# Optimization experiments

Hardware: AMD Instinct MI355X
Metric: run time of the kernel (lower is better)

## Reference

```python
import jax, jax.numpy as jnp
import numpy as np

V, E = 100000, 128
B, Q, D = 512, 32, 256
K_NUM, SIGMA, EXACT_SIGMA = 21, 0.1, 0.001
EPS = 1e-8


def _kernel_params():
    # faithful to source (including the sigma/exact_sigma swap at the call site)
    l_mu = [1.0]
    bin_size = 2.0 / (K_NUM - 1)
    l_mu.append(1 - bin_size / 2)
    for j in range(1, K_NUM - 1):
        l_mu.append(l_mu[j] - bin_size)
    mus = sorted(l_mu)
    # kernel_sigmas(n, sigma=exact_sigma, exact_sigma=sigma) due to swapped call
    sig_list = [SIGMA] + [EXACT_SIGMA] * (K_NUM - 1)
    sigmas = sorted(sig_list)[::-1]
    return (jnp.asarray(mus, dtype=jnp.float32),
            jnp.asarray(sigmas, dtype=jnp.float32))

MUS, SIGMAS = _kernel_params()


def setup_inputs() -> dict:
    key = jax.random.key(0)
    ks = jax.random.split(key, 11)
    emb = jax.random.normal(ks[0], (V, E), dtype=jnp.float32)
    emb = emb.at[0].set(0.0)  # padding_idx=0
    w1 = jax.random.normal(ks[1], (K_NUM, 10), dtype=jnp.float32) / np.sqrt(K_NUM)
    b1 = jax.random.normal(ks[2], (10,), dtype=jnp.float32) * 0.01
    w2 = jax.random.normal(ks[3], (10, 5), dtype=jnp.float32) / np.sqrt(10)
    b2 = jax.random.normal(ks[4], (5,), dtype=jnp.float32) * 0.01
    w3 = jax.random.normal(ks[5], (5, 1), dtype=jnp.float32) / np.sqrt(5)
    b3 = jax.random.normal(ks[6], (1,), dtype=jnp.float32) * 0.01
    query1 = jax.random.randint(ks[7], (B, Q), 0, V, dtype=jnp.int64 if jax.config.jax_enable_x64 else jnp.int32)
    doc1 = jax.random.randint(ks[8], (B, D), 0, V, dtype=query1.dtype)
    query2 = jax.random.randint(ks[9], (B, Q), 0, V, dtype=query1.dtype)
    doc2 = jax.random.randint(ks[10], (B, D), 0, V, dtype=query1.dtype)
    return {"emb": emb, "w1": w1, "b1": b1, "w2": w2, "b2": b2,
            "w3": w3, "b3": b3, "query1": query1, "doc1": doc1,
            "query2": query2, "doc2": doc2}


def _l2norm(x):
    n = jnp.linalg.norm(x, axis=-1, keepdims=True)
    return x / jnp.maximum(n, EPS)


def _predict(emb, w1, b1, w2, b2, w3, b3, q_idx, d_idx):
    q_idx = jnp.clip(q_idx, 0, V - 1)
    d_idx = jnp.clip(d_idx, 0, V - 1)
    qn = _l2norm(emb[q_idx])            # [B,Q,E]
    dn = _l2norm(emb[d_idx])            # [B,D,E]
    mm = jnp.einsum('bqe,bde->bqd', qn, dn)  # cosine matching matrix [B,Q,D]
    # soft-histogram Gaussian kernel pooling: [B,Q,D,K]
    phi = jnp.exp(-0.5 * (mm[..., None] - MUS) ** 2 / SIGMAS ** 2)
    k_out = jnp.log1p(phi.sum(axis=2)).sum(axis=1)  # [B,K]
    x = jax.nn.relu(k_out) @ w1 + b1
    x = jax.nn.relu(x) @ w2 + b2
    x = jax.nn.relu(x) @ w3 + b3
    return x  # [B,1]


def reference(emb, w1, b1, w2, b2, w3, b3, query1, doc1, query2, doc2):
    logits_1 = _predict(emb, w1, b1, w2, b2, w3, b3, query1, doc1)
    logits_2 = _predict(emb, w1, b1, w2, b2, w3, b3, query2, doc2)
    return jax.nn.sigmoid(logits_1 - logits_2)
```

## Files before the change

kernel.cpp:

```cpp
#include <hip/hip_runtime.h>
#include <math.h>

#define V_SIZE 100000
#define E_DIM  128
#define B_SIZE 512
#define Q_LEN  32
#define D_LEN  256
#define K_NUM  21


typedef _Float16 half8_t  __attribute__((ext_vector_type(8)));
typedef float    float4_t __attribute__((ext_vector_type(4)));

__global__ __launch_bounds__(256, 4) void knrm_main(
    const float* __restrict__ emb,
    const int* __restrict__ q1, const int* __restrict__ d1,
    const int* __restrict__ q2, const int* __restrict__ d2,
    const float* __restrict__ w1, const float* __restrict__ b1,
    const float* __restrict__ w2, const float* __restrict__ b2,
    const float* __restrict__ w3, const float* __restrict__ b3,
    float* __restrict__ logits)
{
    const int b    = blockIdx.x;
    const int pair = blockIdx.y;
    const int t    = threadIdx.x;
    const int* __restrict__ qidx = pair ? q2 : q1;
    const int* __restrict__ didx = pair ? d2 : d1;

    __shared__ half8_t AfH[2][4][64];
    __shared__ half8_t AfL[2][4][64];
    __shared__ float rnq[Q_LEN];
    __shared__ float phis[Q_LEN][22];
    __shared__ float ko[K_NUM];

    const int lane = t & 63;
    const int w    = t >> 6;
    const int quad = lane >> 4;
    const int l15  = lane & 15;

    for (int i = t; i < Q_LEN * 22; i += 256) ((float*)phis)[i] = 0.f;

    {
        const int qr = t >> 3;
        const int qc = t & 7;
        int qi = qidx[b * Q_LEN + qr];
        qi = min(max(qi, 0), V_SIZE - 1);
        const float4* src = (const float4*)(emb + (size_t)qi * E_DIM) + qc * 4;
        float4 v0 = src[0], v1 = src[1], v2 = src[2], v3 = src[3];
        float fv[16] = {v0.x,v0.y,v0.z,v0.w, v1.x,v1.y,v1.z,v1.w,
                        v2.x,v2.y,v2.z,v2.w, v3.x,v3.y,v3.z,v3.w};
        float ss = 0.f;
        half8_t h0, h1, l0, l1;
        #pragma unroll
        for (int j = 0; j < 8; ++j) {
            ss = fmaf(fv[j], fv[j], ss);
            _Float16 h = (_Float16)fv[j];
            h0[j] = h; l0[j] = (_Float16)(fv[j] - (float)h);
        }
        #pragma unroll
        for (int j = 0; j < 8; ++j) {
            ss = fmaf(fv[8 + j], fv[8 + j], ss);
            _Float16 h = (_Float16)fv[8 + j];
            h1[j] = h; l1[j] = (_Float16)(fv[8 + j] - (float)h);
        }
        const int qt  = qr >> 4;
        const int lr  = qr & 15;
        const int s   = qc >> 1;
        const int qd0 = (qc & 1) * 2;
        AfH[qt][s][qd0 * 16 + lr]       = h0;
        AfH[qt][s][(qd0 + 1) * 16 + lr] = h1;
        AfL[qt][s][qd0 * 16 + lr]       = l0;
        AfL[qt][s][(qd0 + 1) * 16 + lr] = l1;
        ss += __shfl_xor(ss, 1, 8);
        ss += __shfl_xor(ss, 2, 8);
        ss += __shfl_xor(ss, 4, 8);
        if (qc == 0) rnq[qr] = 1.0f / fmaxf(sqrtf(ss), 1e-8f);
    }
    __syncthreads();

    float rnqv[8];
    #pragma unroll
    for (int i = 0; i < 8; ++i) rnqv[i] = rnq[(i >> 2) * 16 + quad * 4 + (i & 3)];

    const float cc0 = -0.5f / (0.1f * 0.1f);
    const float ccs = -0.5f / (0.001f * 0.001f);
    float breg[8] = {0.f,0.f,0.f,0.f,0.f,0.f,0.f,0.f};

    int dix[4];
    #pragma unroll
    for (int c = 0; c < 4; ++c) {
        int di = didx[b * D_LEN + w * 64 + c * 16 + l15];
        dix[c] = min(max(di, 0), V_SIZE - 1);
    }

    half8_t bh[4], bl[4];
    float rnd;

    auto convert = [&](const float4* v) {
        float ss = 0.f;
        #pragma unroll
        for (int s = 0; s < 4; ++s) {
            float f[8] = {v[2*s].x, v[2*s].y, v[2*s].z, v[2*s].w,
                          v[2*s+1].x, v[2*s+1].y, v[2*s+1].z, v[2*s+1].w};
            half8_t h, l;
            #pragma unroll
            for (int j = 0; j < 8; ++j) {
                ss = fmaf(f[j], f[j], ss);
                _Float16 hh = (_Float16)f[j];
                h[j] = hh; l[j] = (_Float16)(f[j] - (float)hh);
            }
            bh[s] = h; bl[s] = l;
        }
        ss += __shfl_xor(ss, 16);
        ss += __shfl_xor(ss, 32);
        rnd = 1.0f / fmaxf(sqrtf(ss), 1e-8f);
    };

    {
        const float4* dr = (const float4*)(emb + (size_t)dix[0] * E_DIM) + quad * 2;
        float4 cur[8];
        #pragma unroll
        for (int s = 0; s < 4; ++s) { cur[2*s] = dr[s*8]; cur[2*s+1] = dr[s*8+1]; }
        convert(cur);
    }

    #pragma unroll
    for (int c = 0; c < 4; ++c) {
        float4 nx[8];
        if (c < 3) {
            const float4* dr = (const float4*)(emb + (size_t)dix[c+1] * E_DIM) + quad * 2;
            #pragma unroll
            for (int s = 0; s < 4; ++s) { nx[2*s] = dr[s*8]; nx[2*s+1] = dr[s*8+1]; }
        }

        float4_t acc0 = {0.f,0.f,0.f,0.f}, acc1 = {0.f,0.f,0.f,0.f};
        #pragma unroll
        for (int s = 0; s < 4; ++s) {
            half8_t a0h = AfH[0][s][lane], a0l = AfL[0][s][lane];
            half8_t a1h = AfH[1][s][lane], a1l = AfL[1][s][lane];
            acc0 = __builtin_amdgcn_mfma_f32_16x16x32_f16(a0h, bh[s], acc0, 0, 0, 0);
            acc1 = __builtin_amdgcn_mfma_f32_16x16x32_f16(a1h, bh[s], acc1, 0, 0, 0);
            acc0 = __builtin_amdgcn_mfma_f32_16x16x32_f16(a0l, bh[s], acc0, 0, 0, 0);
            acc1 = __builtin_amdgcn_mfma_f32_16x16x32_f16(a1l, bh[s], acc1, 0, 0, 0);
            acc0 = __builtin_amdgcn_mfma_f32_16x16x32_f16(a0h, bl[s], acc0, 0, 0, 0);
            acc1 = __builtin_amdgcn_mfma_f32_16x16x32_f16(a1h, bl[s], acc1, 0, 0, 0);
        }

        #pragma unroll
        for (int qt = 0; qt < 2; ++qt) {
            const float4_t acc = qt ? acc1 : acc0;
            #pragma unroll
            for (int r = 0; r < 4; ++r) {
                const float mm = acc[r] * rnqv[qt*4 + r] * rnd;
                const float x0 = mm + 0.95f;
                breg[qt*4 + r] += __expf(x0 * x0 * cc0);
                float g = rintf((mm + 0.85f) * 10.f);
                g = fminf(fmaxf(g, 0.f), 18.f);
                float mu = fmaf(g, 0.1f, -0.85f);
                int ks = (int)g + 1;
                if (mm > 0.975f) { mu = 1.0f; ks = 20; }
                const float xs = mm - mu;
                const float es = __expf(xs * xs * ccs);
                if (es > 0.f) atomicAdd(&phis[qt*16 + quad*4 + r][ks], es);
            }
        }

        if (c < 3) convert(nx);
    }

    #pragma unroll
    for (int i = 0; i < 8; ++i) {
        float v = breg[i];
        v += __shfl_xor(v, 1, 16);
        v += __shfl_xor(v, 2, 16);
        v += __shfl_xor(v, 4, 16);
        v += __shfl_xor(v, 8, 16);
        if (l15 == 0) atomicAdd(&phis[(i >> 2) * 16 + quad * 4 + (i & 3)][0], v);
    }
    __syncthreads();

    for (int p = t; p < K_NUM * Q_LEN; p += 256) {
        const int q = p & 31;
        const int k = p >> 5;
        float l = log1pf(phis[q][k]);
        l += __shfl_xor(l, 1, 32);
        l += __shfl_xor(l, 2, 32);
        l += __shfl_xor(l, 4, 32);
        l += __shfl_xor(l, 8, 32);
        l += __shfl_xor(l, 16, 32);
        if (q == 0) ko[k] = l;
    }
    __syncthreads();

    if (t == 0) {
        float x1v[10];
        #pragma unroll
        for (int i = 0; i < 10; ++i) {
            float s = b1[i];
            for (int k = 0; k < K_NUM; ++k) {
                float v = ko[k] > 0.f ? ko[k] : 0.f;
                s = fmaf(v, w1[k * 10 + i], s);
            }
            x1v[i] = s;
        }
        float x2v[5];
        #pragma unroll
        for (int i = 0; i < 5; ++i) {
            float s = b2[i];
            #pragma unroll
            for (int k = 0; k < 10; ++k) {
                float v = x1v[k] > 0.f ? x1v[k] : 0.f;
                s = fmaf(v, w2[k * 5 + i], s);
            }
            x2v[i] = s;
        }
        float s3 = b3[0];
        #pragma unroll
        for (int k = 0; k < 5; ++k) {
            float v = x2v[k] > 0.f ? x2v[k] : 0.f;
            s3 = fmaf(v, w3[k], s3);
        }
        logits[pair * B_SIZE + b] = s3;
    }
}

__global__ void knrm_final(const float* __restrict__ logits, float* __restrict__ out)
{
    const int b = blockIdx.x * blockDim.x + threadIdx.x;
    if (b < B_SIZE) {
        const float dl = logits[b] - logits[B_SIZE + b];
        out[b] = 1.0f / (1.0f + __expf(-dl));
    }
}

extern "C" void kernel_launch(void* const* d_in, const int* in_sizes, int n_in,
                              void* d_out, int out_size, void* d_ws, size_t ws_size,
                              hipStream_t stream)
{
    const float* emb = (const float*)d_in[0];
    const float* w1  = (const float*)d_in[1];
    const float* b1  = (const float*)d_in[2];
    const float* w2  = (const float*)d_in[3];
    const float* b2  = (const float*)d_in[4];
    const float* w3  = (const float*)d_in[5];
    const float* b3  = (const float*)d_in[6];
    const int*   q1  = (const int*)d_in[7];
    const int*   d1  = (const int*)d_in[8];
    const int*   q2  = (const int*)d_in[9];
    const int*   d2  = (const int*)d_in[10];

    float* logits = (float*)d_ws;
    float* out    = (float*)d_out;

    dim3 grid(B_SIZE, 2);
    knrm_main<<<grid, 256, 0, stream>>>(emb, q1, d1, q2, d2,
                                        w1, b1, w2, b2, w3, b3, logits);
    knrm_final<<<(B_SIZE + 255) / 256, 256, 0, stream>>>(logits, out);
}
```

Measured before the change: 124.9 us.

## Fuse both pairs and the sigmoid into one 512-thread kernel

Merges the two per-pair blocks into a single 512-thread block per batch row, so that both logits are computed together and the sigmoid difference is applied in-kernel. This removes the second kernel launch and the round trip through the logits workspace. It also issues the query and first document embedding gathers before the LDS zeroing and conversion, which lets the gather latency overlap with setup work. In exchange the block needs twice the shared memory and threads, which may reduce scheduling flexibility and occupancy.

```diff
diff --git a/kernel.cpp b/kernel.cpp
--- a/kernel.cpp
+++ b/kernel.cpp
@@ -12,41 +12,57 @@
 typedef _Float16 half8_t  __attribute__((ext_vector_type(8)));
 typedef float    float4_t __attribute__((ext_vector_type(4)));
 
-__global__ __launch_bounds__(256, 4) void knrm_main(
+__global__ __launch_bounds__(512, 4) void knrm_fused(
     const float* __restrict__ emb,
     const int* __restrict__ q1, const int* __restrict__ d1,
     const int* __restrict__ q2, const int* __restrict__ d2,
     const float* __restrict__ w1, const float* __restrict__ b1,
     const float* __restrict__ w2, const float* __restrict__ b2,
     const float* __restrict__ w3, const float* __restrict__ b3,
-    float* __restrict__ logits)
+    float* __restrict__ out)
 {
     const int b    = blockIdx.x;
-    const int pair = blockIdx.y;
     const int t    = threadIdx.x;
+    const int tl   = t & 255;
+    const int pair = t >> 8;
+
     const int* __restrict__ qidx = pair ? q2 : q1;
     const int* __restrict__ didx = pair ? d2 : d1;
 
-    __shared__ half8_t AfH[2][4][64];
-    __shared__ half8_t AfL[2][4][64];
-    __shared__ float rnq[Q_LEN];
-    __shared__ float phis[Q_LEN][22];
-    __shared__ float ko[K_NUM];
+    __shared__ half8_t AfH[2][2][4][64];
+    __shared__ half8_t AfL[2][2][4][64];
+    __shared__ float rnq[2][Q_LEN];
+    __shared__ float phis[2][Q_LEN][22];
+    __shared__ float ko[2][K_NUM];
+    __shared__ float logitL[2];
 
     const int lane = t & 63;
-    const int w    = t >> 6;
+    const int w    = tl >> 6;
     const int quad = lane >> 4;
     const int l15  = lane & 15;
 
-    for (int i = t; i < Q_LEN * 22; i += 256) ((float*)phis)[i] = 0.f;
+    const int qr = tl >> 3;
+    const int qc = tl & 7;
+    int qi = qidx[b * Q_LEN + qr];
+    int dix[4];
+    #pragma unroll
+    for (int c = 0; c < 4; ++c) {
+        int di = didx[b * D_LEN + w * 64 + c * 16 + l15];
+        dix[c] = min(max(di, 0), V_SIZE - 1);
+    }
+    qi = min(max(qi, 0), V_SIZE - 1);
+
+    const float4* src = (const float4*)(emb + (size_t)qi * E_DIM) + qc * 4;
+    float4 v0 = src[0], v1 = src[1], v2 = src[2], v3 = src[3];
+
+    const float4* dr0 = (const float4*)(emb + (size_t)dix[0] * E_DIM) + quad * 2;
+    float4 cur[8];
+    #pragma unroll
+    for (int s = 0; s < 4; ++s) { cur[2*s] = dr0[s*8]; cur[2*s+1] = dr0[s*8+1]; }
+
+    for (int i = tl; i < Q_LEN * 22; i += 256) ((float*)phis[pair])[i] = 0.f;
 
     {
-        const int qr = t >> 3;
-        const int qc = t & 7;
-        int qi = qidx[b * Q_LEN + qr];
-        qi = min(max(qi, 0), V_SIZE - 1);
-        const float4* src = (const float4*)(emb + (size_t)qi * E_DIM) + qc * 4;
-        float4 v0 = src[0], v1 = src[1], v2 = src[2], v3 = src[3];
         float fv[16] = {v0.x,v0.y,v0.z,v0.w, v1.x,v1.y,v1.z,v1.w,
                         v2.x,v2.y,v2.z,v2.w, v3.x,v3.y,v3.z,v3.w};
         float ss = 0.f;
@@ -67,30 +83,14 @@
         const int lr  = qr & 15;
         const int s   = qc >> 1;
         const int qd0 = (qc & 1) * 2;
-        AfH[qt][s][qd0 * 16 + lr]       = h0;
-        AfH[qt][s][(qd0 + 1) * 16 + lr] = h1;
-        AfL[qt][s][qd0 * 16 + lr]       = l0;
-        AfL[qt][s][(qd0 + 1) * 16 + lr] = l1;
+        AfH[pair][qt][s][qd0 * 16 + lr]       = h0;
+        AfH[pair][qt][s][(qd0 + 1) * 16 + lr] = h1;
+        AfL[pair][qt][s][qd0 * 16 + lr]       = l0;
+        AfL[pair][qt][s][(qd0 + 1) * 16 + lr] = l1;
         ss += __shfl_xor(ss, 1, 8);
         ss += __shfl_xor(ss, 2, 8);
         ss += __shfl_xor(ss, 4, 8);
-        if (qc == 0) rnq[qr] = 1.0f / fmaxf(sqrtf(ss), 1e-8f);
-    }
-    __syncthreads();
-
-    float rnqv[8];
-    #pragma unroll
-    for (int i = 0; i < 8; ++i) rnqv[i] = rnq[(i >> 2) * 16 + quad * 4 + (i & 3)];
-
-    const float cc0 = -0.5f / (0.1f * 0.1f);
-    const float ccs = -0.5f / (0.001f * 0.001f);
-    float breg[8] = {0.f,0.f,0.f,0.f,0.f,0.f,0.f,0.f};
-
-    int dix[4];
-    #pragma unroll
-    for (int c = 0; c < 4; ++c) {
-        int di = didx[b * D_LEN + w * 64 + c * 16 + l15];
-        dix[c] = min(max(di, 0), V_SIZE - 1);
+        if (qc == 0) rnq[pair][qr] = 1.0f / fmaxf(sqrtf(ss), 1e-8f);
     }
 
     half8_t bh[4], bl[4];
@@ -116,13 +116,18 @@
         rnd = 1.0f / fmaxf(sqrtf(ss), 1e-8f);
     };
 
-    {
-        const float4* dr = (const float4*)(emb + (size_t)dix[0] * E_DIM) + quad * 2;
-        float4 cur[8];
-        #pragma unroll
-        for (int s = 0; s < 4; ++s) { cur[2*s] = dr[s*8]; cur[2*s+1] = dr[s*8+1]; }
-        convert(cur);
-    }
+    convert(cur);
+
+    __syncthreads();
+
+    float rnqv[8];
+    #pragma unroll
+    for (int i = 0; i < 8; ++i)
+        rnqv[i] = rnq[pair][(i >> 2) * 16 + quad * 4 + (i & 3)];
+
+    const float cc0 = -0.5f / (0.1f * 0.1f);
+    const float ccs = -0.5f / (0.001f * 0.001f);
+    float breg[8] = {0.f,0.f,0.f,0.f,0.f,0.f,0.f,0.f};
 
     #pragma unroll
     for (int c = 0; c < 4; ++c) {
@@ -136,8 +141,8 @@
         float4_t acc0 = {0.f,0.f,0.f,0.f}, acc1 = {0.f,0.f,0.f,0.f};
         #pragma unroll
         for (int s = 0; s < 4; ++s) {
-            half8_t a0h = AfH[0][s][lane], a0l = AfL[0][s][lane];
-            half8_t a1h = AfH[1][s][lane], a1l = AfL[1][s][lane];
+            half8_t a0h = AfH[pair][0][s][lane], a0l = AfL[pair][0][s][lane];
+            half8_t a1h = AfH[pair][1][s][lane], a1l = AfL[pair][1][s][lane];
             acc0 = __builtin_amdgcn_mfma_f32_16x16x32_f16(a0h, bh[s], acc0, 0, 0, 0);
             acc1 = __builtin_amdgcn_mfma_f32_16x16x32_f16(a1h, bh[s], acc1, 0, 0, 0);
             acc0 = __builtin_amdgcn_mfma_f32_16x16x32_f16(a0l, bh[s], acc0, 0, 0, 0);
@@ -161,7 +166,7 @@
                 if (mm > 0.975f) { mu = 1.0f; ks = 20; }
                 const float xs = mm - mu;
                 const float es = __expf(xs * xs * ccs);
-                if (es > 0.f) atomicAdd(&phis[qt*16 + quad*4 + r][ks], es);
+                if (es > 0.f) atomicAdd(&phis[pair][qt*16 + quad*4 + r][ks], es);
             }
         }
 
@@ -175,30 +180,30 @@
         v += __shfl_xor(v, 2, 16);
         v += __shfl_xor(v, 4, 16);
         v += __shfl_xor(v, 8, 16);
-        if (l15 == 0) atomicAdd(&phis[(i >> 2) * 16 + quad * 4 + (i & 3)][0], v);
-    }
-    __syncthreads();
-
-    for (int p = t; p < K_NUM * Q_LEN; p += 256) {
+        if (l15 == 0) atomicAdd(&phis[pair][(i >> 2) * 16 + quad * 4 + (i & 3)][0], v);
+    }
+    __syncthreads();
+
+    for (int p = tl; p < K_NUM * Q_LEN; p += 256) {
         const int q = p & 31;
         const int k = p >> 5;
-        float l = log1pf(phis[q][k]);
+        float l = log1pf(phis[pair][q][k]);
         l += __shfl_xor(l, 1, 32);
         l += __shfl_xor(l, 2, 32);
         l += __shfl_xor(l, 4, 32);
         l += __shfl_xor(l, 8, 32);
         l += __shfl_xor(l, 16, 32);
-        if (q == 0) ko[k] = l;
-    }
-    __syncthreads();
-
-    if (t == 0) {
+        if (q == 0) ko[pair][k] = l;
+    }
+    __syncthreads();
+
+    if (tl == 0) {
         float x1v[10];
         #pragma unroll
         for (int i = 0; i < 10; ++i) {
             float s = b1[i];
             for (int k = 0; k < K_NUM; ++k) {
-                float v = ko[k] > 0.f ? ko[k] : 0.f;
+                float v = ko[pair][k] > 0.f ? ko[pair][k] : 0.f;
                 s = fmaf(v, w1[k * 10 + i], s);
             }
             x1v[i] = s;
@@ -220,15 +225,12 @@
             float v = x2v[k] > 0.f ? x2v[k] : 0.f;
             s3 = fmaf(v, w3[k], s3);
         }
-        logits[pair * B_SIZE + b] = s3;
-    }
-}
-
-__global__ void knrm_final(const float* __restrict__ logits, float* __restrict__ out)
-{
-    const int b = blockIdx.x * blockDim.x + threadIdx.x;
-    if (b < B_SIZE) {
-        const float dl = logits[b] - logits[B_SIZE + b];
+        logitL[pair] = s3;
+    }
+    __syncthreads();
+
+    if (t == 0) {
+        const float dl = logitL[0] - logitL[1];
         out[b] = 1.0f / (1.0f + __expf(-dl));
     }
 }
@@ -249,11 +251,9 @@
     const int*   q2  = (const int*)d_in[9];
     const int*   d2  = (const int*)d_in[10];
 
-    float* logits = (float*)d_ws;
-    float* out    = (float*)d_out;
-
-    dim3 grid(B_SIZE, 2);
-    knrm_main<<<grid, 256, 0, stream>>>(emb, q1, d1, q2, d2,
-                                        w1, b1, w2, b2, w3, b3, logits);
-    knrm_final<<<(B_SIZE + 255) / 256, 256, 0, stream>>>(logits, out);
+    float* out = (float*)d_out;
+    (void)d_ws; (void)ws_size;
+
+    knrm_fused<<<dim3(B_SIZE), 512, 0, stream>>>(emb, q1, d1, q2, d2,
+                                                 w1, b1, w2, b2, w3, b3, out);
 }
```

Result: no change. 122.6 us (-1.8%).
